# Optimization experiments

Measured on AMD Instinct MI355X. Metric: run time of the kernel, lower is better.

## Reference

```python
import jax, jax.numpy as jnp
import numpy as np

B, C, H, W = 8, 96, 512, 96  # W == w_size (required by the view semantics)
EPS = 1e-5


def setup_inputs() -> dict:
    key = jax.random.key(0)
    ks = jax.random.split(key, 3)
    x = jax.random.normal(ks[0], (B, C, H, W), dtype=jnp.float32)
    bn_gamma = jnp.ones((C,), jnp.float32)
    bn_beta = jnp.zeros((C,), jnp.float32)
    bn_mean = jnp.zeros((C,), jnp.float32)   # BatchNorm running mean (eval mode)
    bn_var = jnp.ones((C,), jnp.float32)     # BatchNorm running var  (eval mode)
    qkv_w = jax.random.normal(ks[1], (3 * C, C), jnp.float32) * (1.0 / np.sqrt(C))
    qkv_b = jnp.zeros((3 * C,), jnp.float32)
    return {"x": x, "bn_gamma": bn_gamma, "bn_beta": bn_beta,
            "bn_mean": bn_mean, "bn_var": bn_var,
            "qkv_w": qkv_w, "qkv_b": qkv_b}


def reference(x, bn_gamma, bn_beta, bn_mean, bn_var, qkv_w, qkv_b):
    # BatchNorm2d (eval-mode affine normalize), fused scale/shift per channel
    inv = (bn_gamma / jnp.sqrt(bn_var + EPS))[:, None, None]
    xn = (x - bn_mean[:, None, None]) * inv + bn_beta[:, None, None]
    # 1x1 conv QKV projection: [b,c,h,w] -> [b,3c,h,w]
    qkv = jnp.einsum('bchw,oc->bohw', xn, qkv_w) + qkv_b[None, :, None, None]
    q, k, v = jnp.split(qkv, 3, axis=1)  # each [b,c,h,w]
    # per-row attention over the width axis (w == w_size)
    qp = jnp.transpose(q, (0, 2, 3, 1))  # [b,h,w,c]
    kp = jnp.transpose(k, (0, 2, 3, 1))  # [b,h,w,c]
    vp = jnp.transpose(v, (0, 2, 3, 1))  # [b,h,w,c]
    score = jnp.einsum('bhqc,bhkc->bhqk', qp, kp)  # [b,h,w,w]
    attn = jax.nn.softmax(score, axis=-1)
    xt = jnp.einsum('bhqk,bhkc->bhqc', attn, vp)   # [b,h,w,c]
    out = jnp.transpose(xt, (0, 3, 1, 2)) + x       # residual add, [b,c,h,w]
    return out
```

## Files before the change

kernel.cpp:

```cpp
#include <hip/hip_runtime.h>

#define C_ 96
#define H_ 512
#define W_ 96
#define HW_ 49152
#define CHW_ 4718592
#define PIT 104
#define REG 9984

typedef _Float16 f16x8 __attribute__((ext_vector_type(8)));
typedef _Float16 f16x4 __attribute__((ext_vector_type(4)));
typedef _Float16 f16x2 __attribute__((ext_vector_type(2)));
typedef float    f32x4 __attribute__((ext_vector_type(4)));
typedef int      i32x4 __attribute__((ext_vector_type(4)));

#define MFMA16 __builtin_amdgcn_mfma_f32_16x16x32_f16

#define BAR() do { __builtin_amdgcn_sched_barrier(0); \
                   asm volatile("s_waitcnt lgkmcnt(0)" ::: "memory"); \
                   __builtin_amdgcn_s_barrier(); \
                   __builtin_amdgcn_sched_barrier(0); } while (0)

__global__ void prep_kernel(const float* __restrict__ wq,
                            const float* __restrict__ gamma,
                            const float* __restrict__ beta,
                            const float* __restrict__ mean,
                            const float* __restrict__ var,
                            const float* __restrict__ qkvb,
                            _Float16* __restrict__ whf,
                            float* __restrict__ bprime)
{
    int i = blockIdx.x * 256 + threadIdx.x;
    if (i < 3 * C_ * C_) {
        int c = i % C_;
        float iv = gamma[c] * rsqrtf(var[c] + 1e-5f);
        whf[i] = (_Float16)(wq[i] * iv);
    }
    if (i < 3 * C_) {
        float acc = qkvb[i];
        for (int c = 0; c < C_; ++c) {
            float iv = gamma[c] * rsqrtf(var[c] + 1e-5f);
            acc += wq[i * C_ + c] * (beta[c] - mean[c] * iv);
        }
        bprime[i] = acc;
    }
}

__global__ __launch_bounds__(384, 5) void attn_kernel(
    const float* __restrict__ x,
    const _Float16* __restrict__ wqkv,
    const float* __restrict__ bprime,
    float* __restrict__ out)
{
    __shared__ __align__(16) _Float16 smem[2 * REG];
    _Float16* XV = smem;
    _Float16* KP = smem + REG;

    const int tid  = threadIdx.x;
    const int ws   = tid >> 6;
    const int lane = tid & 63;
    const int q4   = lane >> 4;
    const int n16  = lane & 15;
    const int w0   = 16 * ws + 4 * q4;

    const int bh = blockIdx.x;
    const size_t base = (size_t)(bh >> 9) * CHW_ + (size_t)(bh & 511) * W_;

    f32x4 xr[6];
    #pragma unroll
    for (int t = 0; t < 6; ++t)
        xr[t] = *(const f32x4*)(x + base + (size_t)(16 * t + n16) * HW_ + w0);
    #pragma unroll
    for (int t = 0; t < 6; ++t) {
        const int c = 16 * t + n16;
        #pragma unroll
        for (int r = 0; r < 4; ++r)
            XV[(w0 + r) * PIT + c] = (_Float16)xr[t][r];
    }
    BAR();

    f32x4 qac[6];
    #pragma unroll
    for (int ot = 0; ot < 6; ++ot)
        qac[ot] = *(const f32x4*)(bprime + 16 * ot + 4 * q4);
    #pragma unroll
    for (int kk = 0; kk < 3; ++kk) {
        const f16x8 bfr = *(const f16x8*)(XV + (16 * ws + n16) * PIT + 32 * kk + 8 * q4);
        #pragma unroll
        for (int ot = 0; ot < 6; ++ot) {
            const f16x8 afr = *(const f16x8*)(wqkv + (16 * ot + n16) * 96 + 32 * kk + 8 * q4);
            qac[ot] = MFMA16(afr, bfr, qac[ot], 0, 0, 0);
        }
    }
    int pq[6][2];
    #pragma unroll
    for (int ot = 0; ot < 6; ++ot) {
        #pragma unroll
        for (int jj = 0; jj < 2; ++jj) {
            f16x2 h;
            h[0] = (_Float16)qac[ot][2 * jj];
            h[1] = (_Float16)qac[ot][2 * jj + 1];
            pq[ot][jj] = __builtin_bit_cast(int, h);
        }
    }
    const int srcA = ((q4 & 1) << 5) | n16;
    const int srcB = srcA + 16;
    f16x8 qf[3];
    #pragma unroll
    for (int kk = 0; kk < 3; ++kk) {
        const int a0 = __shfl(pq[2 * kk][0], srcA), a1 = __shfl(pq[2 * kk][1], srcA);
        const int a2 = __shfl(pq[2 * kk][0], srcB), a3 = __shfl(pq[2 * kk][1], srcB);
        const int b0 = __shfl(pq[2 * kk + 1][0], srcA), b1 = __shfl(pq[2 * kk + 1][1], srcA);
        const int b2 = __shfl(pq[2 * kk + 1][0], srcB), b3 = __shfl(pq[2 * kk + 1][1], srcB);
        i32x4 u;
        u[0] = (q4 < 2) ? a0 : b0;
        u[1] = (q4 < 2) ? a1 : b1;
        u[2] = (q4 < 2) ? a2 : b2;
        u[3] = (q4 < 2) ? a3 : b3;
        qf[kk] = __builtin_bit_cast(f16x8, u);
    }

    f32x4 kac[6];
    {
        const f32x4 bb = *(const f32x4*)(bprime + 96 + 16 * ws + 4 * q4);
        #pragma unroll
        for (int nt = 0; nt < 6; ++nt) kac[nt] = bb;
    }
    #pragma unroll
    for (int kk = 0; kk < 3; ++kk) {
        const f16x8 afr = *(const f16x8*)(wqkv + (96 + 16 * ws + n16) * 96 + 32 * kk + 8 * q4);
        #pragma unroll
        for (int nt = 0; nt < 6; ++nt) {
            const f16x8 bfr = *(const f16x8*)(XV + (16 * nt + n16) * PIT + 32 * kk + 8 * q4);
            kac[nt] = MFMA16(afr, bfr, kac[nt], 0, 0, 0);
        }
    }
    #pragma unroll
    for (int nt = 0; nt < 6; ++nt) {
        f16x4 pk;
        #pragma unroll
        for (int r = 0; r < 4; ++r) pk[r] = (_Float16)kac[nt][r];
        *(f16x4*)(KP + (16 * nt + n16) * PIT + 16 * ws + 4 * q4) = pk;
    }

    f32x4 vac[6];
    {
        const float bv = bprime[192 + 16 * ws + n16];
        #pragma unroll
        for (int nt = 0; nt < 6; ++nt) vac[nt] = f32x4{bv, bv, bv, bv};
    }
    #pragma unroll
    for (int kk = 0; kk < 3; ++kk) {
        const f16x8 wb = *(const f16x8*)(wqkv + (192 + 16 * ws + n16) * 96 + 32 * kk + 8 * q4);
        #pragma unroll
        for (int nt = 0; nt < 6; ++nt) {
            const f16x8 xa = *(const f16x8*)(XV + (16 * nt + n16) * PIT + 32 * kk + 8 * q4);
            vac[nt] = MFMA16(xa, wb, vac[nt], 0, 0, 0);
        }
    }
    BAR();

    #pragma unroll
    for (int nt = 0; nt < 6; ++nt) {
        f16x4 pk;
        #pragma unroll
        for (int r = 0; r < 4; ++r) pk[r] = (_Float16)vac[nt][r];
        *(f16x4*)(XV + (16 * ws + n16) * PIT + 16 * nt + 4 * q4) = pk;
    }

    f32x4 sacc[6];
    #pragma unroll
    for (int nt = 0; nt < 6; ++nt) sacc[nt] = f32x4{0.f, 0.f, 0.f, 0.f};
    #pragma unroll
    for (int kk = 0; kk < 3; ++kk) {
        #pragma unroll
        for (int nt = 0; nt < 6; ++nt) {
            const f16x8 ka = *(const f16x8*)(KP + (16 * nt + n16) * PIT + 32 * kk + 8 * q4);
            sacc[nt] = MFMA16(ka, qf[kk], sacc[nt], 0, 0, 0);
        }
    }
    float mr0 = sacc[0][0], mr1 = sacc[0][1], mr2 = sacc[0][2], mr3 = sacc[0][3];
    #pragma unroll
    for (int nt = 1; nt < 6; ++nt) {
        mr0 = fmaxf(mr0, sacc[nt][0]); mr1 = fmaxf(mr1, sacc[nt][1]);
        mr2 = fmaxf(mr2, sacc[nt][2]); mr3 = fmaxf(mr3, sacc[nt][3]);
    }
    float m = fmaxf(fmaxf(mr0, mr1), fmaxf(mr2, mr3));
    m = fmaxf(m, __shfl_xor(m, 16));
    m = fmaxf(m, __shfl_xor(m, 32));
    float sr0 = 0.f, sr1 = 0.f, sr2 = 0.f, sr3 = 0.f;
    #pragma unroll
    for (int nt = 0; nt < 6; ++nt) {
        sacc[nt][0] = __expf(sacc[nt][0] - m); sr0 += sacc[nt][0];
        sacc[nt][1] = __expf(sacc[nt][1] - m); sr1 += sacc[nt][1];
        sacc[nt][2] = __expf(sacc[nt][2] - m); sr2 += sacc[nt][2];
        sacc[nt][3] = __expf(sacc[nt][3] - m); sr3 += sacc[nt][3];
    }
    float s = (sr0 + sr1) + (sr2 + sr3);
    s += __shfl_xor(s, 16);
    s += __shfl_xor(s, 32);
    const float pinv = 1.0f / s;

    BAR();

    #pragma unroll
    for (int nt = 0; nt < 6; ++nt) {
        f16x4 pk;
        #pragma unroll
        for (int r = 0; r < 4; ++r) pk[r] = (_Float16)(sacc[nt][r] * pinv);
        *(f16x4*)(KP + (16 * ws + n16) * PIT + 16 * nt + 4 * q4) = pk;
    }

    f32x4 oacc[6];
    #pragma unroll
    for (int nt = 0; nt < 6; ++nt) oacc[nt] = f32x4{0.f, 0.f, 0.f, 0.f};
    #pragma unroll
    for (int kk = 0; kk < 3; ++kk) {
        const f16x8 pa = *(const f16x8*)(KP + (16 * ws + n16) * PIT + 32 * kk + 8 * q4);
        #pragma unroll
        for (int nt = 0; nt < 6; ++nt) {
            const f16x8 vb = *(const f16x8*)(XV + (16 * nt + n16) * PIT + 32 * kk + 8 * q4);
            oacc[nt] = MFMA16(pa, vb, oacc[nt], 0, 0, 0);
        }
    }

    #pragma unroll
    for (int nt = 0; nt < 6; ++nt) {
        f32x4 o4;
        #pragma unroll
        for (int r = 0; r < 4; ++r) o4[r] = oacc[nt][r] + xr[nt][r];
        *(f32x4*)(out + base + (size_t)(16 * nt + n16) * HW_ + w0) = o4;
    }
}

extern "C" void kernel_launch(void* const* d_in, const int* in_sizes, int n_in,
                              void* d_out, int out_size, void* d_ws, size_t ws_size,
                              hipStream_t stream)
{
    const float* x     = (const float*)d_in[0];
    const float* gamma = (const float*)d_in[1];
    const float* beta  = (const float*)d_in[2];
    const float* mean  = (const float*)d_in[3];
    const float* var   = (const float*)d_in[4];
    const float* qkvw  = (const float*)d_in[5];
    const float* qkvb  = (const float*)d_in[6];
    float* out = (float*)d_out;

    _Float16* whf    = (_Float16*)d_ws;
    float*    bprime = (float*)((char*)d_ws + 55296);

    prep_kernel<<<108, 256, 0, stream>>>(qkvw, gamma, beta, mean, var, qkvb, whf, bprime);
    attn_kernel<<<4096, 384, 0, stream>>>(x, whf, bprime, out);
}
```

Measured before the change: 343.2 us.

## Fold Q/K projections into precomputed Wq^T Wk matrix and defer V projection

Precomputes A = Wq^T Wk (with BN scales folded) and a bias vector in a new prep kernel, so scores become x^T A x plus a per-key term, and no longer need separate Q and K projections. The V projection is applied after attention (P·X then Wv), with bias added once because softmax rows sum to one. This removes the K/V staging through shared memory and some barriers, and stores x in both layouts in LDS. In exchange the output is written with scalar, strided stores, and x is reloaded per element for the residual, which may cost memory efficiency. Dropping the query-side bias term is valid because it is constant across each softmax row.

```diff
diff --git a/kernel.cpp b/kernel.cpp
--- a/kernel.cpp
+++ b/kernel.cpp
@@ -46,66 +46,48 @@
     }
 }
 
-__global__ __launch_bounds__(384, 5) void attn_kernel(
-    const float* __restrict__ x,
-    const _Float16* __restrict__ wqkv,
-    const float* __restrict__ bprime,
-    float* __restrict__ out)
-{
-    __shared__ __align__(16) _Float16 smem[2 * REG];
-    _Float16* XV = smem;
-    _Float16* KP = smem + REG;
-
-    const int tid  = threadIdx.x;
-    const int ws   = tid >> 6;
-    const int lane = tid & 63;
-    const int q4   = lane >> 4;
-    const int n16  = lane & 15;
-    const int w0   = 16 * ws + 4 * q4;
-
-    const int bh = blockIdx.x;
-    const size_t base = (size_t)(bh >> 9) * CHW_ + (size_t)(bh & 511) * W_;
-
-    f32x4 xr[6];
-    #pragma unroll
-    for (int t = 0; t < 6; ++t)
-        xr[t] = *(const f32x4*)(x + base + (size_t)(16 * t + n16) * HW_ + w0);
-    #pragma unroll
-    for (int t = 0; t < 6; ++t) {
-        const int c = 16 * t + n16;
-        #pragma unroll
-        for (int r = 0; r < 4; ++r)
-            XV[(w0 + r) * PIT + c] = (_Float16)xr[t][r];
-    }
-    BAR();
-
-    f32x4 qac[6];
-    #pragma unroll
-    for (int ot = 0; ot < 6; ++ot)
-        qac[ot] = *(const f32x4*)(bprime + 16 * ot + 4 * q4);
-    #pragma unroll
-    for (int kk = 0; kk < 3; ++kk) {
-        const f16x8 bfr = *(const f16x8*)(XV + (16 * ws + n16) * PIT + 32 * kk + 8 * q4);
-        #pragma unroll
-        for (int ot = 0; ot < 6; ++ot) {
-            const f16x8 afr = *(const f16x8*)(wqkv + (16 * ot + n16) * 96 + 32 * kk + 8 * q4);
-            qac[ot] = MFMA16(afr, bfr, qac[ot], 0, 0, 0);
-        }
-    }
+__global__ void prep2_kernel(const float* __restrict__ wq,
+                             const float* __restrict__ gamma,
+                             const float* __restrict__ var,
+                             const float* __restrict__ bprime,
+                             _Float16* __restrict__ atm,
+                             float* __restrict__ g0)
+{
+    int i = blockIdx.x * 256 + threadIdx.x;
+    if (i >= 9216) return;
+    int c = i / 96, cp = i % 96;
+    float ivc  = gamma[c]  * rsqrtf(var[c]  + 1e-5f);
+    float ivcp = gamma[cp] * rsqrtf(var[cp] + 1e-5f);
+    float acc = 0.f;
+    #pragma unroll 4
+    for (int o = 0; o < 96; ++o)
+        acc += wq[o * 96 + cp] * wq[(96 + o) * 96 + c];
+    atm[c * 96 + cp] = (_Float16)(acc * ivc * ivcp);
+    if (cp == 0) {
+        float a2 = 0.f;
+        #pragma unroll 4
+        for (int o = 0; o < 96; ++o)
+            a2 += bprime[o] * wq[(96 + o) * 96 + c];
+        g0[c] = a2 * ivc;
+    }
+}
+
+__device__ __forceinline__ void xchg(const f32x4 v[6], float scale,
+                                     int q4, int n16, f16x8 fr[3])
+{
     int pq[6][2];
     #pragma unroll
-    for (int ot = 0; ot < 6; ++ot) {
+    for (int nt = 0; nt < 6; ++nt) {
         #pragma unroll
         for (int jj = 0; jj < 2; ++jj) {
             f16x2 h;
-            h[0] = (_Float16)qac[ot][2 * jj];
-            h[1] = (_Float16)qac[ot][2 * jj + 1];
-            pq[ot][jj] = __builtin_bit_cast(int, h);
+            h[0] = (_Float16)(v[nt][2 * jj] * scale);
+            h[1] = (_Float16)(v[nt][2 * jj + 1] * scale);
+            pq[nt][jj] = __builtin_bit_cast(int, h);
         }
     }
     const int srcA = ((q4 & 1) << 5) | n16;
     const int srcB = srcA + 16;
-    f16x8 qf[3];
     #pragma unroll
     for (int kk = 0; kk < 3; ++kk) {
         const int a0 = __shfl(pq[2 * kk][0], srcA), a1 = __shfl(pq[2 * kk][1], srcA);
@@ -117,68 +99,80 @@
         u[1] = (q4 < 2) ? a1 : b1;
         u[2] = (q4 < 2) ? a2 : b2;
         u[3] = (q4 < 2) ? a3 : b3;
-        qf[kk] = __builtin_bit_cast(f16x8, u);
-    }
-
-    f32x4 kac[6];
+        fr[kk] = __builtin_bit_cast(f16x8, u);
+    }
+}
+
+__global__ __launch_bounds__(384, 5) void attn_kernel(
+    const float* __restrict__ x,
+    const _Float16* __restrict__ whf,
+    const _Float16* __restrict__ atm,
+    const float* __restrict__ g0,
+    const float* __restrict__ bprime,
+    float* __restrict__ out)
+{
+    __shared__ __align__(16) _Float16 smem[2 * REG];
+    _Float16* XN  = smem;
+    _Float16* XNT = smem + REG;
+
+    const int tid  = threadIdx.x;
+    const int ws   = tid >> 6;
+    const int lane = tid & 63;
+    const int q4   = lane >> 4;
+    const int n16  = lane & 15;
+    const int w0   = 16 * ws + 4 * q4;
+    const int qrow = 16 * ws + n16;
+
+    const int bh = blockIdx.x;
+    const size_t base = (size_t)(bh >> 9) * CHW_ + (size_t)(bh & 511) * W_;
+
     {
-        const f32x4 bb = *(const f32x4*)(bprime + 96 + 16 * ws + 4 * q4);
-        #pragma unroll
-        for (int nt = 0; nt < 6; ++nt) kac[nt] = bb;
-    }
-    #pragma unroll
-    for (int kk = 0; kk < 3; ++kk) {
-        const f16x8 afr = *(const f16x8*)(wqkv + (96 + 16 * ws + n16) * 96 + 32 * kk + 8 * q4);
+        f32x4 xr[6];
+        #pragma unroll
+        for (int t = 0; t < 6; ++t)
+            xr[t] = *(const f32x4*)(x + base + (size_t)(16 * t + n16) * HW_ + w0);
+        #pragma unroll
+        for (int t = 0; t < 6; ++t) {
+            const int c = 16 * t + n16;
+            f16x4 pk;
+            #pragma unroll
+            for (int r = 0; r < 4; ++r) pk[r] = (_Float16)xr[t][r];
+            *(f16x4*)(XNT + c * PIT + w0) = pk;
+            #pragma unroll
+            for (int r = 0; r < 4; ++r)
+                XN[(w0 + r) * PIT + c] = (_Float16)xr[t][r];
+        }
+    }
+    BAR();
+
+    f32x4 gac[6];
+    #pragma unroll
+    for (int nt = 0; nt < 6; ++nt)
+        gac[nt] = *(const f32x4*)(g0 + 16 * nt + 4 * q4);
+    #pragma unroll
+    for (int kk = 0; kk < 3; ++kk) {
+        const f16x8 bfr = *(const f16x8*)(XN + qrow * PIT + 32 * kk + 8 * q4);
         #pragma unroll
         for (int nt = 0; nt < 6; ++nt) {
-            const f16x8 bfr = *(const f16x8*)(XV + (16 * nt + n16) * PIT + 32 * kk + 8 * q4);
-            kac[nt] = MFMA16(afr, bfr, kac[nt], 0, 0, 0);
-        }
-    }
-    #pragma unroll
-    for (int nt = 0; nt < 6; ++nt) {
-        f16x4 pk;
-        #pragma unroll
-        for (int r = 0; r < 4; ++r) pk[r] = (_Float16)kac[nt][r];
-        *(f16x4*)(KP + (16 * nt + n16) * PIT + 16 * ws + 4 * q4) = pk;
-    }
-
-    f32x4 vac[6];
-    {
-        const float bv = bprime[192 + 16 * ws + n16];
-        #pragma unroll
-        for (int nt = 0; nt < 6; ++nt) vac[nt] = f32x4{bv, bv, bv, bv};
-    }
-    #pragma unroll
-    for (int kk = 0; kk < 3; ++kk) {
-        const f16x8 wb = *(const f16x8*)(wqkv + (192 + 16 * ws + n16) * 96 + 32 * kk + 8 * q4);
+            const f16x8 afr = *(const f16x8*)(atm + (16 * nt + n16) * 96 + 32 * kk + 8 * q4);
+            gac[nt] = MFMA16(afr, bfr, gac[nt], 0, 0, 0);
+        }
+    }
+    f16x8 gf[3];
+    xchg(gac, 1.0f, q4, n16, gf);
+
+    f32x4 sacc[6];
+    #pragma unroll
+    for (int nt = 0; nt < 6; ++nt) sacc[nt] = f32x4{0.f, 0.f, 0.f, 0.f};
+    #pragma unroll
+    for (int kk = 0; kk < 3; ++kk) {
         #pragma unroll
         for (int nt = 0; nt < 6; ++nt) {
-            const f16x8 xa = *(const f16x8*)(XV + (16 * nt + n16) * PIT + 32 * kk + 8 * q4);
-            vac[nt] = MFMA16(xa, wb, vac[nt], 0, 0, 0);
-        }
-    }
-    BAR();
-
-    #pragma unroll
-    for (int nt = 0; nt < 6; ++nt) {
-        f16x4 pk;
-        #pragma unroll
-        for (int r = 0; r < 4; ++r) pk[r] = (_Float16)vac[nt][r];
-        *(f16x4*)(XV + (16 * ws + n16) * PIT + 16 * nt + 4 * q4) = pk;
-    }
-
-    f32x4 sacc[6];
-    #pragma unroll
-    for (int nt = 0; nt < 6; ++nt) sacc[nt] = f32x4{0.f, 0.f, 0.f, 0.f};
-    #pragma unroll
-    for (int kk = 0; kk < 3; ++kk) {
-        #pragma unroll
-        for (int nt = 0; nt < 6; ++nt) {
-            const f16x8 ka = *(const f16x8*)(KP + (16 * nt + n16) * PIT + 32 * kk + 8 * q4);
-            sacc[nt] = MFMA16(ka, qf[kk], sacc[nt], 0, 0, 0);
-        }
-    }
+            const f16x8 afr = *(const f16x8*)(XN + (16 * nt + n16) * PIT + 32 * kk + 8 * q4);
+            sacc[nt] = MFMA16(afr, gf[kk], sacc[nt], 0, 0, 0);
+        }
+    }
+
     float mr0 = sacc[0][0], mr1 = sacc[0][1], mr2 = sacc[0][2], mr3 = sacc[0][3];
     #pragma unroll
     for (int nt = 1; nt < 6; ++nt) {
@@ -201,36 +195,49 @@
     s += __shfl_xor(s, 32);
     const float pinv = 1.0f / s;
 
-    BAR();
-
-    #pragma unroll
-    for (int nt = 0; nt < 6; ++nt) {
-        f16x4 pk;
-        #pragma unroll
-        for (int r = 0; r < 4; ++r) pk[r] = (_Float16)(sacc[nt][r] * pinv);
-        *(f16x4*)(KP + (16 * ws + n16) * PIT + 16 * nt + 4 * q4) = pk;
-    }
+    f16x8 pa[3];
+    xchg(sacc, pinv, q4, n16, pa);
+
+    float xv[6][4];
+    #pragma unroll
+    for (int ot = 0; ot < 6; ++ot)
+        #pragma unroll
+        for (int r = 0; r < 4; ++r)
+            xv[ot][r] = x[base + (size_t)(16 * ot + 4 * q4 + r) * HW_ + qrow];
+
+    f32x4 zac[6];
+    #pragma unroll
+    for (int nt = 0; nt < 6; ++nt) zac[nt] = f32x4{0.f, 0.f, 0.f, 0.f};
+    #pragma unroll
+    for (int kk = 0; kk < 3; ++kk) {
+        #pragma unroll
+        for (int nt = 0; nt < 6; ++nt) {
+            const f16x8 afr = *(const f16x8*)(XNT + (16 * nt + n16) * PIT + 32 * kk + 8 * q4);
+            zac[nt] = MFMA16(afr, pa[kk], zac[nt], 0, 0, 0);
+        }
+    }
+    f16x8 zf[3];
+    xchg(zac, 1.0f, q4, n16, zf);
 
     f32x4 oacc[6];
     #pragma unroll
-    for (int nt = 0; nt < 6; ++nt) oacc[nt] = f32x4{0.f, 0.f, 0.f, 0.f};
-    #pragma unroll
-    for (int kk = 0; kk < 3; ++kk) {
-        const f16x8 pa = *(const f16x8*)(KP + (16 * ws + n16) * PIT + 32 * kk + 8 * q4);
-        #pragma unroll
-        for (int nt = 0; nt < 6; ++nt) {
-            const f16x8 vb = *(const f16x8*)(XV + (16 * nt + n16) * PIT + 32 * kk + 8 * q4);
-            oacc[nt] = MFMA16(pa, vb, oacc[nt], 0, 0, 0);
-        }
-    }
-
-    #pragma unroll
-    for (int nt = 0; nt < 6; ++nt) {
-        f32x4 o4;
-        #pragma unroll
-        for (int r = 0; r < 4; ++r) o4[r] = oacc[nt][r] + xr[nt][r];
-        *(f32x4*)(out + base + (size_t)(16 * nt + n16) * HW_ + w0) = o4;
-    }
+    for (int ot = 0; ot < 6; ++ot)
+        oacc[ot] = *(const f32x4*)(bprime + 192 + 16 * ot + 4 * q4);
+    #pragma unroll
+    for (int kk = 0; kk < 3; ++kk) {
+        #pragma unroll
+        for (int ot = 0; ot < 6; ++ot) {
+            const f16x8 afr = *(const f16x8*)(whf + (192 + 16 * ot + n16) * 96 + 32 * kk + 8 * q4);
+            oacc[ot] = MFMA16(afr, zf[kk], oacc[ot], 0, 0, 0);
+        }
+    }
+
+    #pragma unroll
+    for (int ot = 0; ot < 6; ++ot)
+        #pragma unroll
+        for (int r = 0; r < 4; ++r)
+            out[base + (size_t)(16 * ot + 4 * q4 + r) * HW_ + qrow] =
+                oacc[ot][r] + xv[ot][r];
 }
 
 extern "C" void kernel_launch(void* const* d_in, const int* in_sizes, int n_in,
@@ -248,7 +255,10 @@
 
     _Float16* whf    = (_Float16*)d_ws;
     float*    bprime = (float*)((char*)d_ws + 55296);
+    _Float16* atm    = (_Float16*)((char*)d_ws + 56448);
+    float*    g0v    = (float*)((char*)d_ws + 74880);
 
     prep_kernel<<<108, 256, 0, stream>>>(qkvw, gamma, beta, mean, var, qkvb, whf, bprime);
-    attn_kernel<<<4096, 384, 0, stream>>>(x, whf, bprime, out);
-}
+    prep2_kernel<<<36, 256, 0, stream>>>(qkvw, gamma, var, bprime, atm, g0v);
+    attn_kernel<<<4096, 384, 0, stream>>>(x, whf, atm, g0v, bprime, out);
+}
```

Measured after the change: 366.1 us. +6.7%, slower.
